# Kernel optimization log

Measured on AMD Instinct MI355X. Metric: run time of the kernel, lower is better.

## Reference

```python
import jax, jax.numpy as jnp
import numpy as np

TAU = 2.0       # spikingjelly LIFNode default
V_TH = 1.0      # v_threshold default
ALPHA = 2.0     # surrogate.ATan default alpha

@jax.custom_vjp
def atan_spike(x):
    # Heaviside forward, ATan surrogate gradient backward
    return (x >= 0.0).astype(x.dtype)

def _atan_fwd(x):
    return atan_spike(x), x

def _atan_bwd(x, g):
    return (g * (ALPHA / 2.0) / (1.0 + (jnp.pi / 2.0 * ALPHA * x) ** 2),)

atan_spike.defvjp(_atan_fwd, _atan_bwd)

def lif_scan(cur):
    # cur: [T, ...]; LIF with decay_input=True, hard reset to v_reset=0
    def step(v, c):
        v = v + (c - v) / TAU          # charge with decayed input
        s = atan_spike(v - V_TH)       # fire
        v = (1.0 - s) * v              # hard reset (v_reset = 0)
        return v, s
    v0 = jnp.zeros(cur.shape[1:], cur.dtype)
    _, spikes = jax.lax.scan(step, v0, cur)
    return spikes

def setup_inputs() -> dict:
    key = jax.random.key(0)
    k1, k2 = jax.random.split(key, 2)
    T, B, D = 2048, 32, 512
    x = jax.random.normal(k1, (T, B, D), dtype=jnp.float32)
    W = jax.random.normal(k2, (D, D), dtype=jnp.float32) / np.sqrt(D).astype(np.float32)
    b = jnp.zeros((D,), dtype=jnp.float32)
    return {"x": x, "W": W, "b": b}

def reference(x, W, b):
    # x: [T, B, D]
    xs = jnp.stack([x, jnp.flip(x, axis=0)], axis=2)          # [T, B, 2, D]
    cur = jnp.einsum('tbkd,ed->tbke', xs, W) + b              # Linear (y = x W^T + b)
    s = lif_scan(cur)                                          # [T, B, 2, D] spikes
    return s[:, :, 0, :] + jnp.flip(s[:, :, 1, :], axis=0)    # [T, B, D]
```

## Files before the change

kernel.cpp:

```cpp
#include <hip/hip_runtime.h>
#include <cstddef>
#include <cstdint>

#define T_LEN 2048
#define B_SZ  32
#define D_SZ  512
#define BD    (B_SZ * D_SZ)

#define BM   128
#define BN   128

typedef const __attribute__((address_space(1))) uint32_t* gas1_t;
typedef __attribute__((address_space(3))) uint32_t* las3_t;

__global__ __launch_bounds__(256) void gemm8x8_kernel(
    const float* __restrict__ A,
    const float* __restrict__ W,
    const float* __restrict__ bias,
    float* __restrict__ Y)
{
#pragma clang fp contract(off)
  __shared__ float As[2][BM * 16];
  __shared__ float Bs[2][BN * 16];

  const int tid = threadIdx.x;
  const int tx  = tid & 15;
  const int ty  = tid >> 4;
  const int cB  = (tx >> 1) & 3;

  const int nwg  = (int)(gridDim.x * gridDim.y);
  const int orig = (int)(blockIdx.y * gridDim.x + blockIdx.x);
  const int q    = nwg >> 3, r = nwg & 7;
  const int xcd  = orig & 7, loc = orig >> 3;
  const int tix  = (xcd < r ? xcd * (q + 1) : r * (q + 1) + (xcd - r) * q) + loc;
  const int m0   = (tix >> 2) * BM;
  const int n0   = (tix & 3) * BN;

  const int lane  = tid & 63;
  const int wid   = tid >> 6;
  const int rloc  = lane >> 2;
  const int qA4   = ((lane & 3) << 2);
  const int qB4   = (((lane & 3) ^ ((rloc >> 1) & 3)) << 2);
  const int s0    = 2 * wid, s1 = 2 * wid + 1;
  const int oS0   = s0 * 256, oS1 = s1 * 256;
  const float* gA0 = A + (size_t)(m0 + s0 * 16 + rloc) * D_SZ + qA4;
  const float* gA1 = A + (size_t)(m0 + s1 * 16 + rloc) * D_SZ + qA4;
  const float* gB0 = W + (size_t)(n0 + s0 * 16 + rloc) * D_SZ + qB4;
  const float* gB1 = W + (size_t)(n0 + s1 * 16 + rloc) * D_SZ + qB4;

#define STAGE(BUF, KOFF)                                                      \
  do {                                                                        \
    __builtin_amdgcn_global_load_lds((gas1_t)(const void*)(gA0 + (KOFF)),     \
                                     (las3_t)(void*)(&As[BUF][oS0]), 16, 0, 0);\
    __builtin_amdgcn_global_load_lds((gas1_t)(const void*)(gA1 + (KOFF)),     \
                                     (las3_t)(void*)(&As[BUF][oS1]), 16, 0, 0);\
    __builtin_amdgcn_global_load_lds((gas1_t)(const void*)(gB0 + (KOFF)),     \
                                     (las3_t)(void*)(&Bs[BUF][oS0]), 16, 0, 0);\
    __builtin_amdgcn_global_load_lds((gas1_t)(const void*)(gB1 + (KOFF)),     \
                                     (las3_t)(void*)(&Bs[BUF][oS1]), 16, 0, 0);\
  } while (0)

  float acc[8][8];
#pragma unroll
  for (int i = 0; i < 8; ++i)
#pragma unroll
    for (int j = 0; j < 8; ++j) acc[i][j] = 0.0f;

  STAGE(0, 0);
  __syncthreads();

#pragma unroll 1
  for (int kc = 0; kc < 32; ++kc) {
    const int cur = kc & 1;
    if (kc + 1 < 32) STAGE(cur ^ 1, (kc + 1) * 16);

    const float* asb = &As[cur][0] + ty * 16;
    const float* bsb = &Bs[cur][0] + tx * 16;
#pragma unroll
    for (int kq = 0; kq < 4; ++kq) {
      const int aq = kq << 2;
      const int bq = ((kq ^ cB) & 3) << 2;
      const float4 a0 = *(const float4*)&asb[0 * 256 + aq];
      const float4 a1 = *(const float4*)&asb[1 * 256 + aq];
      const float4 a2 = *(const float4*)&asb[2 * 256 + aq];
      const float4 a3 = *(const float4*)&asb[3 * 256 + aq];
      const float4 a4 = *(const float4*)&asb[4 * 256 + aq];
      const float4 a5 = *(const float4*)&asb[5 * 256 + aq];
      const float4 a6 = *(const float4*)&asb[6 * 256 + aq];
      const float4 a7 = *(const float4*)&asb[7 * 256 + aq];
#pragma unroll
      for (int j = 0; j < 8; ++j) {
        const float4 b = *(const float4*)&bsb[j * 256 + bq];
#define FMA4(I, AV)                                                           \
        acc[I][j] = fmaf(AV.x, b.x, acc[I][j]);                               \
        acc[I][j] = fmaf(AV.y, b.y, acc[I][j]);                               \
        acc[I][j] = fmaf(AV.z, b.z, acc[I][j]);                               \
        acc[I][j] = fmaf(AV.w, b.w, acc[I][j]);
        FMA4(0, a0) FMA4(1, a1) FMA4(2, a2) FMA4(3, a3)
        FMA4(4, a4) FMA4(5, a5) FMA4(6, a6) FMA4(7, a7)
#undef FMA4
      }
    }
    __syncthreads();
  }
#undef STAGE

#pragma unroll
  for (int i = 0; i < 8; ++i) {
    const int m = m0 + ty + 16 * i;
#pragma unroll
    for (int j = 0; j < 8; ++j) {
      const int n = n0 + tx + 16 * j;
      Y[(size_t)m * D_SZ + n] = acc[i][j] + bias[n];
    }
  }
}

#define CHK  16
#define CLEN 128

__global__ __launch_bounds__(64) void scan_chunk_kernel(
    const float* __restrict__ Y,
    float* __restrict__ out)
{
#pragma clang fp contract(off)
  const int idx = blockIdx.x * 64 + threadIdx.x;
  const int c   = blockIdx.y;
  const int t0  = c * CLEN;
  float ca[32], cb[32];
  uint32_t sf0, sf1, sf2, sf3, sb0, sb1, sb2, sb3;
  float v;

#define LD(R, TB)                                                             \
  _Pragma("unroll")                                                           \
  for (int j = 0; j < 32; ++j) R[j] = Y[(size_t)((TB) + j) * BD + idx];

#define FCH(R, W)                                                             \
  {                                                                           \
    uint32_t w_ = 0;                                                          \
    _Pragma("unroll")                                                         \
    for (int j = 0; j < 32; ++j) {                                            \
      v = v + (R[j] - v) * 0.5f;                                              \
      const bool s = (v - 1.0f) >= 0.0f;                                      \
      w_ |= (uint32_t)s << j;                                                 \
      v = s ? 0.0f : v;                                                       \
    }                                                                         \
    W = w_;                                                                   \
  }

#define BCH(R, W)                                                             \
  {                                                                           \
    uint32_t w_ = 0;                                                          \
    _Pragma("unroll")                                                         \
    for (int j = 31; j >= 0; --j) {                                           \
      v = v + (R[j] - v) * 0.5f;                                              \
      const bool s = (v - 1.0f) >= 0.0f;                                      \
      w_ |= (uint32_t)s << j;                                                 \
      v = s ? 0.0f : v;                                                       \
    }                                                                         \
    W = w_;                                                                   \
  }

  uint32_t wdump;

  v = 0.0f;
  if (c > 0) {
    LD(ca, t0 - 64)
    LD(cb, t0 - 32)
    FCH(ca, wdump)
    LD(ca, t0)
    FCH(cb, wdump)
  } else {
    LD(ca, t0)
  }
  LD(cb, t0 + 32)  FCH(ca, sf0)
  LD(ca, t0 + 64)  FCH(cb, sf1)
  LD(cb, t0 + 96)  FCH(ca, sf2)
                   FCH(cb, sf3)

  v = 0.0f;
  if (c < CHK - 1) {
    LD(ca, t0 + CLEN + 32)
    LD(cb, t0 + CLEN)
    BCH(ca, wdump)
    LD(ca, t0 + 96)
    BCH(cb, wdump)
  } else {
    LD(ca, t0 + 96)
  }
  LD(cb, t0 + 64)  BCH(ca, sb3)
  LD(ca, t0 + 32)  BCH(cb, sb2)
  LD(cb, t0)       BCH(ca, sb1)
                   BCH(cb, sb0)

#define WGRP(SF, SB, G)                                                       \
  _Pragma("unroll")                                                           \
  for (int j = 0; j < 32; ++j)                                                \
    out[(size_t)(t0 + (G) * 32 + j) * BD + idx] =                             \
        (float)(((SF >> j) & 1u) + ((SB >> j) & 1u));
  WGRP(sf0, sb0, 0) WGRP(sf1, sb1, 1) WGRP(sf2, sb2, 2) WGRP(sf3, sb3, 3)

#undef LD
#undef FCH
#undef BCH
#undef WGRP
}

__global__ __launch_bounds__(64) void lif_fwd_kernel(
    const float* __restrict__ Y, float* __restrict__ out,
    int tlen, float* __restrict__ vstate, int carry)
{
#pragma clang fp contract(off)
  const int idx = blockIdx.x * 64 + threadIdx.x;
  float v = carry ? vstate[idx] : 0.0f;
#pragma unroll 16
  for (int t = 0; t < tlen; ++t) {
    const float c = Y[(size_t)t * BD + idx];
    v = v + (c - v) * 0.5f;
    const bool s = (v - 1.0f) >= 0.0f;
    out[(size_t)t * BD + idx] = s ? 1.0f : 0.0f;
    v = s ? 0.0f : v;
  }
  vstate[idx] = v;
}

__global__ __launch_bounds__(64) void lif_bwd_kernel(
    const float* __restrict__ Y, float* __restrict__ out,
    int tlen, float* __restrict__ vstate, int carry)
{
#pragma clang fp contract(off)
  const int idx = blockIdx.x * 64 + threadIdx.x;
  float v = carry ? vstate[idx] : 0.0f;
#pragma unroll 16
  for (int tt = 0; tt < tlen; ++tt) {
    const size_t t = (size_t)(tlen - 1 - tt);
    const float c = Y[t * BD + idx];
    v = v + (c - v) * 0.5f;
    const bool s = (v - 1.0f) >= 0.0f;
    out[t * BD + idx] += s ? 1.0f : 0.0f;
    v = s ? 0.0f : v;
  }
  vstate[idx] = v;
}

extern "C" void kernel_launch(void* const* d_in, const int* in_sizes, int n_in,
                              void* d_out, int out_size, void* d_ws, size_t ws_size,
                              hipStream_t stream)
{
  const float* x = (const float*)d_in[0];
  const float* W = (const float*)d_in[1];
  const float* b = (const float*)d_in[2];
  float* out = (float*)d_out;

  const size_t full_bytes = (size_t)T_LEN * BD * sizeof(float);
  const size_t vbytes     = (size_t)BD * sizeof(float);

  if (ws_size >= full_bytes) {
    float* Y = (float*)d_ws;
    dim3 grid(T_LEN * B_SZ / BM, D_SZ / BN);
    gemm8x8_kernel<<<grid, 256, 0, stream>>>(x, W, b, Y);
    scan_chunk_kernel<<<dim3(BD / 64, CHK), 64, 0, stream>>>(Y, out);
  } else {
    const size_t avail = ws_size > vbytes ? ws_size - vbytes : 0;
    int Tc = T_LEN;
    while (Tc > 4 && (size_t)Tc * BD * sizeof(float) > avail) Tc >>= 1;
    float* Y      = (float*)d_ws;
    float* vstate = (float*)((char*)d_ws + (size_t)Tc * BD * sizeof(float));

    int first = 1;
    for (int t0 = 0; t0 < T_LEN; t0 += Tc) {
      dim3 grid(Tc * B_SZ / BM, D_SZ / BN);
      gemm8x8_kernel<<<grid, 256, 0, stream>>>(x + (size_t)t0 * BD, W, b, Y);
      lif_fwd_kernel<<<BD / 64, 64, 0, stream>>>(Y, out + (size_t)t0 * BD, Tc,
                                                 vstate, first ? 0 : 1);
      first = 0;
    }
    first = 1;
    for (int t0 = T_LEN - Tc; t0 >= 0; t0 -= Tc) {
      dim3 grid(Tc * B_SZ / BM, D_SZ / BN);
      gemm8x8_kernel<<<grid, 256, 0, stream>>>(x + (size_t)t0 * BD, W, b, Y);
      lif_bwd_kernel<<<BD / 64, 64, 0, stream>>>(Y, out + (size_t)t0 * BD, Tc,
                                                 vstate, first ? 0 : 1);
      first = 0;
    }
  }
}
```

Baseline: 676.9 us.

## Triple-buffer GEMM LDS stages with prefetch distance two and swizzle A tiles

The fp32 GEMM moves from a double-buffered loop with a full __syncthreads per K-chunk to a three-buffer ring. Loads are issued two chunks ahead, and each step waits only until the previous stage's loads land (vmcnt(4)) before a single barrier. The A tile now gets an XOR swizzle on its LDS column quads, matching the one B already had, to cut bank conflicts. The inner product is also reordered so the eight B fragments stay in registers while A rows stream through. This costs 50% more LDS and more live registers, which could lower occupancy or cause spills.

```diff
diff --git a/kernel.cpp b/kernel.cpp
--- a/kernel.cpp
+++ b/kernel.cpp
@@ -20,12 +20,13 @@
     float* __restrict__ Y)
 {
 #pragma clang fp contract(off)
-  __shared__ float As[2][BM * 16];
-  __shared__ float Bs[2][BN * 16];
+  __shared__ float As[3][BM * 16];
+  __shared__ float Bs[3][BN * 16];
 
   const int tid = threadIdx.x;
   const int tx  = tid & 15;
   const int ty  = tid >> 4;
+  const int cA  = ty & 3;
   const int cB  = (tx >> 1) & 3;
 
   const int nwg  = (int)(gridDim.x * gridDim.y);
@@ -39,7 +40,7 @@
   const int lane  = tid & 63;
   const int wid   = tid >> 6;
   const int rloc  = lane >> 2;
-  const int qA4   = ((lane & 3) << 2);
+  const int qA4   = (((lane & 3) ^ (rloc & 3)) << 2);
   const int qB4   = (((lane & 3) ^ ((rloc >> 1) & 3)) << 2);
   const int s0    = 2 * wid, s1 = 2 * wid + 1;
   const int oS0   = s0 * 256, oS1 = s1 * 256;
@@ -60,6 +61,42 @@
                                      (las3_t)(void*)(&Bs[BUF][oS1]), 16, 0, 0);\
   } while (0)
 
+#define COMP(BUF)                                                             \
+  {                                                                           \
+    const float* asb = &As[BUF][0];                                           \
+    const float* bsb = &Bs[BUF][0];                                           \
+    _Pragma("unroll")                                                         \
+    for (int kq = 0; kq < 4; ++kq) {                                          \
+      const int bq = ((kq ^ cB) & 3) << 2;                                    \
+      const int aq = ((kq ^ cA) & 3) << 2;                                    \
+      float4 bfr[8];                                                          \
+      _Pragma("unroll")                                                       \
+      for (int j = 0; j < 8; ++j)                                             \
+        bfr[j] = *(const float4*)&bsb[(tx + 16 * j) * 16 + bq];               \
+      _Pragma("unroll")                                                       \
+      for (int i = 0; i < 8; ++i) {                                           \
+        const float4 a = *(const float4*)&asb[(ty + 16 * i) * 16 + aq];       \
+        _Pragma("unroll")                                                     \
+        for (int j = 0; j < 8; ++j) {                                         \
+          acc[i][j] = fmaf(a.x, bfr[j].x, acc[i][j]);                         \
+          acc[i][j] = fmaf(a.y, bfr[j].y, acc[i][j]);                         \
+          acc[i][j] = fmaf(a.z, bfr[j].z, acc[i][j]);                         \
+          acc[i][j] = fmaf(a.w, bfr[j].w, acc[i][j]);                         \
+        }                                                                     \
+      }                                                                       \
+    }                                                                         \
+  }
+
+#define SYNC_CNT4                                                             \
+  do {                                                                        \
+    asm volatile("s_waitcnt vmcnt(4)" ::: "memory");                          \
+    __builtin_amdgcn_s_barrier();                                             \
+    asm volatile("" ::: "memory");                                            \
+  } while (0)
+
+#define BODY(CBUF, SBUF, KOFF)                                                \
+  do { STAGE(SBUF, KOFF); COMP(CBUF); SYNC_CNT4; } while (0)
+
   float acc[8][8];
 #pragma unroll
   for (int i = 0; i < 8; ++i)
@@ -67,42 +104,26 @@
     for (int j = 0; j < 8; ++j) acc[i][j] = 0.0f;
 
   STAGE(0, 0);
-  __syncthreads();
+  STAGE(1, 16);
+  SYNC_CNT4;
 
 #pragma unroll 1
-  for (int kc = 0; kc < 32; ++kc) {
-    const int cur = kc & 1;
-    if (kc + 1 < 32) STAGE(cur ^ 1, (kc + 1) * 16);
-
-    const float* asb = &As[cur][0] + ty * 16;
-    const float* bsb = &Bs[cur][0] + tx * 16;
-#pragma unroll
-    for (int kq = 0; kq < 4; ++kq) {
-      const int aq = kq << 2;
-      const int bq = ((kq ^ cB) & 3) << 2;
-      const float4 a0 = *(const float4*)&asb[0 * 256 + aq];
-      const float4 a1 = *(const float4*)&asb[1 * 256 + aq];
-      const float4 a2 = *(const float4*)&asb[2 * 256 + aq];
-      const float4 a3 = *(const float4*)&asb[3 * 256 + aq];
-      const float4 a4 = *(const float4*)&asb[4 * 256 + aq];
-      const float4 a5 = *(const float4*)&asb[5 * 256 + aq];
-      const float4 a6 = *(const float4*)&asb[6 * 256 + aq];
-      const float4 a7 = *(const float4*)&asb[7 * 256 + aq];
-#pragma unroll
-      for (int j = 0; j < 8; ++j) {
-        const float4 b = *(const float4*)&bsb[j * 256 + bq];
-#define FMA4(I, AV)                                                           \
-        acc[I][j] = fmaf(AV.x, b.x, acc[I][j]);                               \
-        acc[I][j] = fmaf(AV.y, b.y, acc[I][j]);                               \
-        acc[I][j] = fmaf(AV.z, b.z, acc[I][j]);                               \
-        acc[I][j] = fmaf(AV.w, b.w, acc[I][j]);
-        FMA4(0, a0) FMA4(1, a1) FMA4(2, a2) FMA4(3, a3)
-        FMA4(4, a4) FMA4(5, a5) FMA4(6, a6) FMA4(7, a7)
-#undef FMA4
-      }
-    }
-    __syncthreads();
-  }
+  for (int t = 0; t < 10; ++t) {
+    const int kc = 3 * t;
+    BODY(0, 2, (kc + 2) * 16);
+    BODY(1, 0, (kc + 3) * 16);
+    BODY(2, 1, (kc + 4) * 16);
+  }
+
+  COMP(0);
+  asm volatile("s_waitcnt vmcnt(0)" ::: "memory");
+  __builtin_amdgcn_s_barrier();
+  asm volatile("" ::: "memory");
+  COMP(1);
+
+#undef BODY
+#undef SYNC_CNT4
+#undef COMP
 #undef STAGE
 
 #pragma unroll
```

Result: slower. 706.0 us (+4.3%).
